# Optimization experiments

Hardware: AMD Instinct MI355X
Metric: run time of the kernel (lower is better)

The kernel has to match this reference:

```python
import jax, jax.numpy as jnp
import numpy as np
from math import factorial

L_MAX = 3
K = 256
N = 2048


def _cg_coeff(l1, m1, l2, m2, l3, m3):
    # Clebsch-Gordan coefficient <l1 m1 l2 m2 | l3 m3> via the Racah formula.
    if m3 != m1 + m2:
        return 0.0
    pref = ((2 * l3 + 1) * factorial(l3 + l1 - l2) * factorial(l3 - l1 + l2)
            * factorial(l1 + l2 - l3) / factorial(l1 + l2 + l3 + 1)) ** 0.5
    pref *= (factorial(l3 + m3) * factorial(l3 - m3) * factorial(l1 - m1)
             * factorial(l1 + m1) * factorial(l2 - m2) * factorial(l2 + m2)) ** 0.5
    s = 0.0
    for k in range(0, l1 + l2 - l3 + 1):
        d = [k, l1 + l2 - l3 - k, l1 - m1 - k, l2 + m2 - k,
             l3 - l2 + m1 + k, l3 - l1 - m2 + k]
        if min(d) < 0:
            continue
        den = 1.0
        for x in d:
            den *= factorial(x)
        s += (-1.0) ** k / den
    return pref * s


def _cg_tensor(l1, l2, l3):
    out = np.zeros((2 * l1 + 1, 2 * l2 + 1, 2 * l3 + 1), dtype=np.float32)
    for m1 in range(-l1, l1 + 1):
        for m2 in range(-l2, l2 + 1):
            m3 = m1 + m2
            if -l3 <= m3 <= l3:
                out[m1 + l1, m2 + l2, m3 + l3] = _cg_coeff(l1, m1, l2, m2, l3, m3)
    return jnp.asarray(out)


# All (l1, l2) -> l coupling paths allowed by the triangle inequality, l <= L_MAX.
PATHS = {l: [(l1, l2) for l1 in range(L_MAX + 1) for l2 in range(L_MAX + 1)
             if abs(l1 - l2) <= l <= l1 + l2] for l in range(L_MAX + 1)}
CG = {(l1, l2, l): _cg_tensor(l1, l2, l)
      for l in range(L_MAX + 1) for (l1, l2) in PATHS[l]}


def _forward(f1, f2, U, W):
    outs = []
    for l in range(L_MAX + 1):
        # CG tensor product: elementwise over channels k, coupled over (m1, m2) -> m.
        parts = [jnp.einsum('abm,nak,nbk->nmk', CG[(l1, l2, l)], f1[l1], f2[l2])
                 for (l1, l2) in PATHS[l]]
        tp = jnp.concatenate(parts, axis=-1)          # [N, 2l+1, n_paths(l)*K]
        mixed = jnp.einsum('nmc,ck->nmk', tp, U[l])   # U_dict per-l mixing -> [N, 2l+1, K]
        mixed = jnp.einsum('nmk,kj->nmj', mixed, W[l])  # learned per-l linear
        outs.append(f1[l] + mixed)                    # residual
    return tuple(outs)


def setup_inputs() -> dict:
    key = jax.random.key(0)
    ks = jax.random.split(key, 16)
    inp = {}
    for l in range(L_MAX + 1):
        inp[f'f1_l{l}'] = jax.random.normal(ks[l], (N, 2 * l + 1, K), jnp.float32)
        inp[f'f2_l{l}'] = jax.random.normal(ks[4 + l], (N, 2 * l + 1, K), jnp.float32)
        cin = len(PATHS[l]) * K
        inp[f'U_{l}'] = jax.random.normal(ks[8 + l], (cin, K), jnp.float32) / float(np.sqrt(cin))
        inp[f'W_{l}'] = jax.random.normal(ks[12 + l], (K, K), jnp.float32) / float(np.sqrt(K))
    return inp


def reference(f1_l0, f1_l1, f1_l2, f1_l3,
              f2_l0, f2_l1, f2_l2, f2_l3,
              U_0, U_1, U_2, U_3,
              W_0, W_1, W_2, W_3):
    f1 = [f1_l0, f1_l1, f1_l2, f1_l3]
    f2 = [f2_l0, f2_l1, f2_l2, f2_l3]
    U = [U_0, U_1, U_2, U_3]
    W = [W_0, W_1, W_2, W_3]
    return _forward(f1, f2, U, W)
```

## Files before the change

kernel.cpp:

```cpp
#include <hip/hip_runtime.h>
#include <math.h>

typedef __attribute__((ext_vector_type(4))) float f32x4;
typedef __attribute__((ext_vector_type(2))) float f32x2;
typedef __attribute__((ext_vector_type(8))) __bf16 bf16x8;
typedef __attribute__((ext_vector_type(4))) __bf16 bf16x4;
typedef __attribute__((ext_vector_type(2))) __bf16 bf16x2;

__device__ __constant__ int GP_L[34]  = {0,0,0,0, 1,1,1,1,1,1,1,1,1, 2,2,2,2,2,2,2,2,2,2,2, 3,3,3,3,3,3,3,3,3,3};
__device__ __constant__ int GP_L1[34] = {0,1,2,3, 0,1,1,1,2,2,2,3,3, 0,1,1,1,2,2,2,2,3,3,3, 0,1,1,2,2,2,3,3,3,3};
__device__ __constant__ int GP_L2[34] = {0,1,2,3, 1,0,1,2,1,2,3,2,3, 2,1,2,3,0,1,2,3,1,2,3, 3,2,3,1,2,3,0,1,2,3};

__device__ double dfact(int n) { double r = 1.0; for (int i = 2; i <= n; ++i) r *= (double)i; return r; }

__device__ double cg_coeff(int l1, int m1, int l2, int m2, int l3, int m3) {
  if (m3 != m1 + m2) return 0.0;
  double pref = sqrt((2.0 * l3 + 1.0) * dfact(l3 + l1 - l2) * dfact(l3 - l1 + l2)
                     * dfact(l1 + l2 - l3) / dfact(l1 + l2 + l3 + 1));
  pref *= sqrt(dfact(l3 + m3) * dfact(l3 - m3) * dfact(l1 - m1) * dfact(l1 + m1)
               * dfact(l2 - m2) * dfact(l2 + m2));
  double s = 0.0;
  for (int k = 0; k <= l1 + l2 - l3; ++k) {
    int d0 = k, d1 = l1 + l2 - l3 - k, d2 = l1 - m1 - k, d3 = l2 + m2 - k;
    int d4 = l3 - l2 + m1 + k, d5 = l3 - l1 - m2 + k;
    if (d0 < 0 || d1 < 0 || d2 < 0 || d3 < 0 || d4 < 0 || d5 < 0) continue;
    double den = dfact(d0) * dfact(d1) * dfact(d2) * dfact(d3) * dfact(d4) * dfact(d5);
    s += ((k & 1) ? -1.0 : 1.0) / den;
  }
  return pref * s;
}

__global__ __launch_bounds__(256) void prep(
    const float* __restrict__ u0, const float* __restrict__ u1,
    const float* __restrict__ u2, const float* __restrict__ u3,
    const float* __restrict__ w0, const float* __restrict__ w1,
    const float* __restrict__ w2, const float* __restrict__ w3,
    __bf16* __restrict__ Ubf, __bf16* __restrict__ Wt, float* __restrict__ cg) {
  const int bid = blockIdx.x, tid = threadIdx.x;
  if (bid < 2176) {
    long i = (long)bid * 256 + tid;
    const long b1 = 65536, b2 = 212992, b3 = 393216;
    const float* src; long s;
    if (i < b1)      { src = u0; s = i; }
    else if (i < b2) { src = u1; s = i - b1; }
    else if (i < b3) { src = u2; s = i - b2; }
    else             { src = u3; s = i - b3; }
    float4 v = ((const float4*)src)[s];
    bf16x4 o;
    o[0] = (__bf16)v.x; o[1] = (__bf16)v.y; o[2] = (__bf16)v.z; o[3] = (__bf16)v.w;
    ((bf16x4*)Ubf)[i] = o;
  } else if (bid < 3200) {
    int b = bid - 2176;
    int l = b >> 8, j = b & 255;
    const float* W = (l == 0) ? w0 : (l == 1) ? w1 : (l == 2) ? w2 : w3;
    Wt[((long)l << 16) + (j << 8) + tid] = (__bf16)W[(tid << 8) + j];
  } else {
    int idx = (bid - 3200) * 256 + tid;
    if (idx < 34 * 49) {
      int gp = idx / 49, r = idx % 49;
      int m1i = r / 7, m2i = r % 7;
      int l3 = GP_L[gp], l1 = GP_L1[gp], l2 = GP_L2[gp];
      float v = 0.f;
      if (m1i <= 2 * l1 && m2i <= 2 * l2) {
        int m1 = m1i - l1, m2 = m2i - l2, m3 = m1 + m2;
        if (m3 >= -l3 && m3 <= l3) v = (float)cg_coeff(l1, m1, l2, m2, l3, m3);
      }
      cg[idx] = v;
    }
  }
}

struct GemmDesc {
  const __bf16* A[4];
  const __bf16* B[4];
  __bf16*       C[4];
  int start[4];
  int lmap[4];
  int Kd[4];
  int Nc[4];
};

__device__ __forceinline__ void gload_lds16(const void* g, void* l) {
  __builtin_amdgcn_global_load_lds((const __attribute__((address_space(1))) void*)g,
                                   (__attribute__((address_space(3))) void*)l, 16, 0, 0);
}

__device__ void uw_body(const GemmDesc& d, int bid, char* sm) {
  const int tid = threadIdx.x;
  int seg = 0;
  if (bid >= d.start[1]) seg = 1;
  if (bid >= d.start[2]) seg = 2;
  if (bid >= d.start[3]) seg = 3;
  const int l = d.lmap[seg];
  const int rel = bid - d.start[seg];
  const int Kd = d.Kd[l], Nc = d.Nc[l];
  const int nTN = Nc >> 7;
  const int tM = rel / nTN, tN = rel % nTN;

  const int lane = tid & 63, wave = tid >> 6;
  const int wm = (wave >> 1) << 6, wn = (wave & 1) << 6;
  const int lr = lane & 15, lk = (lane >> 4) << 3;

  f32x4 acc[4][4] = {};

  const int r32 = tid >> 3;
  const int sl = ((tid & 7) ^ (r32 & 7)) << 3;
  const __bf16* Ag = d.A[l] + (long)(tM * 128 + r32) * Kd + sl;
  const __bf16* Bg = d.B[l] + (long)(tN * 128 + r32) * Kd + sl;
  char* AsB = sm;
  char* BsB = sm + 16384;

  for (int kt = 0; kt < Kd; kt += 64) {
#pragma unroll
    for (int i = 0; i < 4; ++i) {
      gload_lds16(Ag + (long)i * 32 * Kd + kt, AsB + i * 4096 + tid * 16);
      gload_lds16(Bg + (long)i * 32 * Kd + kt, BsB + i * 4096 + tid * 16);
    }
    __syncthreads();

#pragma unroll
    for (int kk = 0; kk < 64; kk += 32) {
      bf16x8 af[4], bq[4];
#pragma unroll
      for (int mi = 0; mi < 4; ++mi)
        af[mi] = *(const bf16x8*)(AsB + ((wm + mi * 16 + lr) << 7)
                                      + ((((kk + lk) << 1)) ^ ((lr & 7) << 4)));
#pragma unroll
      for (int ni = 0; ni < 4; ++ni)
        bq[ni] = *(const bf16x8*)(BsB + ((wn + ni * 16 + lr) << 7)
                                      + ((((kk + lk) << 1)) ^ ((lr & 7) << 4)));
#pragma unroll
      for (int mi = 0; mi < 4; ++mi)
#pragma unroll
        for (int ni = 0; ni < 4; ++ni)
          acc[mi][ni] = __builtin_amdgcn_mfma_f32_16x16x32_bf16(af[mi], bq[ni], acc[mi][ni], 0, 0, 0);
    }
    __syncthreads();
  }

  const long col0 = (long)tN * 128 + wn + lr;
  const long row0 = (long)tM * 128 + wm + ((lane >> 4) << 2);
#pragma unroll
  for (int mi = 0; mi < 4; ++mi)
#pragma unroll
    for (int j = 0; j < 4; ++j) {
      long r = row0 + mi * 16 + j;
      long base = r * (long)Nc + col0;
#pragma unroll
      for (int ni = 0; ni < 4; ++ni)
        d.C[l][base + ni * 16] = (__bf16)acc[mi][ni][j];
    }
}

#define TPW2(LV, DST, CIN, GOFF, P, L1V, L2V)                                    \
  { f32x2 tp[2 * (LV) + 1];                                                      \
    _Pragma("unroll") for (int m = 0; m <= 2 * (LV); ++m) { tp[m][0] = 0.f; tp[m][1] = 0.f; } \
    const float* cgt = cg + ((GOFF) + (P)) * 49;                                 \
    _Pragma("unroll") for (int a = 0; a <= 2 * (L1V); ++a)                       \
      _Pragma("unroll") for (int b = 0; b <= 2 * (L2V); ++b) {                   \
        const int m = a + b - ((L1V) + (L2V) - (LV));                            \
        if (m >= 0 && m <= 2 * (LV)) {                                           \
          float c = cgt[a * 7 + b];                                              \
          tp[m][0] = fmaf(c, v1[CUM[L1V] + a][0] * v2[CUM[L2V] + b][0], tp[m][0]); \
          tp[m][1] = fmaf(c, v1[CUM[L1V] + a][1] * v2[CUM[L2V] + b][1], tp[m][1]); \
        } }                                                                      \
    __bf16* o = (DST) + (n * (2 * (LV) + 1)) * (CIN) + (P) * 256 + k2;           \
    _Pragma("unroll") for (int m = 0; m <= 2 * (LV); ++m) {                      \
      bf16x2 ov; ov[0] = (__bf16)tp[m][0]; ov[1] = (__bf16)tp[m][1];             \
      *(bf16x2*)(o + (long)m * (CIN)) = ov; } }

template <int LMASK>
__device__ void tp_body(
    const float* __restrict__ f10, const float* __restrict__ f11,
    const float* __restrict__ f12, const float* __restrict__ f13,
    const float* __restrict__ f20, const float* __restrict__ f21,
    const float* __restrict__ f22, const float* __restrict__ f23,
    const float* __restrict__ cg,
    __bf16* __restrict__ A0, __bf16* __restrict__ A1,
    __bf16* __restrict__ A2, __bf16* __restrict__ A3, int bid) {
  const int tid = threadIdx.x;
  const long n = (long)bid * 2 + (tid >> 7);
  const int k2 = (tid & 127) << 1;
  constexpr int CUM[4] = {0, 1, 4, 9};
  const float* f1s[4] = {f10, f11, f12, f13};
  const float* f2s[4] = {f20, f21, f22, f23};

  f32x2 v1[16], v2[16];
#pragma unroll
  for (int l1 = 0; l1 < 4; ++l1) {
    const float* p1 = f1s[l1] + (n * (2 * l1 + 1)) * 256 + k2;
    const float* p2 = f2s[l1] + (n * (2 * l1 + 1)) * 256 + k2;
#pragma unroll
    for (int a = 0; a <= 2 * l1; ++a) {
      v1[CUM[l1] + a] = *(const f32x2*)(p1 + (long)a * 256);
      v2[CUM[l1] + a] = *(const f32x2*)(p2 + (long)a * 256);
    }
  }

  if constexpr (LMASK & 1) {
    TPW2(0, A0, 1024, 0, 0, 0, 0)  TPW2(0, A0, 1024, 0, 1, 1, 1)
    TPW2(0, A0, 1024, 0, 2, 2, 2)  TPW2(0, A0, 1024, 0, 3, 3, 3)
  }
  if constexpr (LMASK & 2) {
    TPW2(1, A1, 2304, 4, 0, 0, 1)  TPW2(1, A1, 2304, 4, 1, 1, 0)
    TPW2(1, A1, 2304, 4, 2, 1, 1)  TPW2(1, A1, 2304, 4, 3, 1, 2)
    TPW2(1, A1, 2304, 4, 4, 2, 1)  TPW2(1, A1, 2304, 4, 5, 2, 2)
    TPW2(1, A1, 2304, 4, 6, 2, 3)  TPW2(1, A1, 2304, 4, 7, 3, 2)
    TPW2(1, A1, 2304, 4, 8, 3, 3)
  }
  if constexpr (LMASK & 4) {
    TPW2(2, A2, 2816, 13, 0, 0, 2)  TPW2(2, A2, 2816, 13, 1, 1, 1)
    TPW2(2, A2, 2816, 13, 2, 1, 2)  TPW2(2, A2, 2816, 13, 3, 1, 3)
    TPW2(2, A2, 2816, 13, 4, 2, 0)  TPW2(2, A2, 2816, 13, 5, 2, 1)
    TPW2(2, A2, 2816, 13, 6, 2, 2)  TPW2(2, A2, 2816, 13, 7, 2, 3)
    TPW2(2, A2, 2816, 13, 8, 3, 1)  TPW2(2, A2, 2816, 13, 9, 3, 2)
    TPW2(2, A2, 2816, 13, 10, 3, 3)
  }
  if constexpr (LMASK & 8) {
    TPW2(3, A3, 2560, 24, 0, 0, 3)  TPW2(3, A3, 2560, 24, 1, 1, 2)
    TPW2(3, A3, 2560, 24, 2, 1, 3)  TPW2(3, A3, 2560, 24, 3, 2, 1)
    TPW2(3, A3, 2560, 24, 4, 2, 2)  TPW2(3, A3, 2560, 24, 5, 2, 3)
    TPW2(3, A3, 2560, 24, 6, 3, 0)  TPW2(3, A3, 2560, 24, 7, 3, 1)
    TPW2(3, A3, 2560, 24, 8, 3, 2)  TPW2(3, A3, 2560, 24, 9, 3, 3)
  }
}

template <int LMASK>
__global__ __launch_bounds__(256) void tp_uw(
    const float* __restrict__ f10, const float* __restrict__ f11,
    const float* __restrict__ f12, const float* __restrict__ f13,
    const float* __restrict__ f20, const float* __restrict__ f21,
    const float* __restrict__ f22, const float* __restrict__ f23,
    const float* __restrict__ cg,
    __bf16* __restrict__ A0, __bf16* __restrict__ A1,
    __bf16* __restrict__ A2, __bf16* __restrict__ A3,
    GemmDesc gd, int nUW) {
  __shared__ __align__(16) char sm[32768];
  const int bid = (int)blockIdx.x;
  if (bid < nUW) {
    uw_body(gd, bid, sm);
  } else if constexpr (LMASK != 0) {
    tp_body<LMASK>(f10, f11, f12, f13, f20, f21, f22, f23, cg,
                   A0, A1, A2, A3, bid - nUW);
  }
}

struct MainDesc {
  const __bf16* A[4];
  const __bf16* B[4];
  float*        C[4];
  const float*  R[4];
  int start[4];
  int lmap[4];
  int cin4[4];
};

__global__ __launch_bounds__(512, 4) void gemm_main(MainDesc d) {
  __shared__ __align__(16) char sm[49152];
  const int tid = threadIdx.x;
  int bid;
  {
    const int cpx = gridDim.x >> 3;
    bid = ((int)blockIdx.x & 7) * cpx + ((int)blockIdx.x >> 3);
  }
  int seg = 0;
  if (bid >= d.start[1]) seg = 1;
  if (bid >= d.start[2]) seg = 2;
  if (bid >= d.start[3]) seg = 3;
  const int l = d.lmap[seg];
  const int tM = bid - d.start[seg];
  const int cin = d.cin4[l];
  const int NT = cin >> 5;

  const __bf16* __restrict__ Aseg = d.A[l] + (long)tM * 128 * cin;
  const __bf16* __restrict__ Bseg = d.B[l];

  const int arow = tid >> 2;
  const int asx = (((tid & 3) ^ ((tid >> 3) & 3)) << 3);
  const int brow0 = tid >> 2;
  const int bsx0 = asx;
  const int brow1 = (512 + tid) >> 2;
  const int bsx1 = (((tid & 3) ^ (((512 + tid) >> 3) & 3)) << 3);

  const int lane = tid & 63, wave = tid >> 6;
  const int wm = (wave >> 2) << 6;
  const int wn = (wave & 3) << 6;
  const int lr = lane & 15;
  const int lslot = lane >> 4;

  f32x4 acc[4][4];
#pragma unroll
  for (int i = 0; i < 4; ++i)
#pragma unroll
    for (int j = 0; j < 4; ++j) { acc[i][j][0]=0.f; acc[i][j][1]=0.f; acc[i][j][2]=0.f; acc[i][j][3]=0.f; }

#define STAGE(s, t)                                                              \
  { char* base_ = sm + (s) * 24576;                                              \
    const long kt_ = (long)(t) << 5;                                             \
    gload_lds16(Aseg + (long)arow * cin + kt_ + asx, base_ + tid * 16);          \
    gload_lds16(Bseg + (long)brow0 * cin + kt_ + bsx0, base_ + 8192 + tid * 16); \
    gload_lds16(Bseg + (long)brow1 * cin + kt_ + bsx1, base_ + 8192 + 8192 + tid * 16); }

  STAGE(0, 0)
  __syncthreads();

  for (int t = 0; t < NT; ++t) {
    const int cur = t & 1;
    if (t + 1 < NT) STAGE(cur ^ 1, t + 1)
    const char* Ab = sm + cur * 24576;
    const char* Bb = Ab + 8192;
    bf16x8 af[4], bq[4];
#pragma unroll
    for (int mi = 0; mi < 4; ++mi) {
      const int row = wm + mi * 16 + lr;
      af[mi] = *(const bf16x8*)(Ab + row * 64 + ((lslot ^ ((row >> 1) & 3)) << 4));
    }
#pragma unroll
    for (int ni = 0; ni < 4; ++ni) {
      const int row = wn + ni * 16 + lr;
      bq[ni] = *(const bf16x8*)(Bb + row * 64 + ((lslot ^ ((row >> 1) & 3)) << 4));
    }
#pragma unroll
    for (int mi = 0; mi < 4; ++mi)
#pragma unroll
      for (int ni = 0; ni < 4; ++ni)
        acc[mi][ni] = __builtin_amdgcn_mfma_f32_16x16x32_bf16(af[mi], bq[ni], acc[mi][ni], 0, 0, 0);
    __syncthreads();
  }
#undef STAGE

  float* __restrict__ Cout = d.C[l];
  const float* __restrict__ Resid = d.R[l];
  const int rb = (lane >> 4) << 2;
#pragma unroll
  for (int mi = 0; mi < 4; ++mi)
#pragma unroll
    for (int j = 0; j < 4; ++j) {
      const long row = (long)tM * 128 + wm + mi * 16 + rb + j;
      const long base = row * 256 + wn + lr;
#pragma unroll
      for (int ni = 0; ni < 4; ++ni)
        Cout[base + ni * 16] = acc[mi][ni][j] + Resid[base + ni * 16];
    }
}

extern "C" void kernel_launch(void* const* d_in, const int* in_sizes, int n_in,
                              void* d_out, int out_size, void* d_ws, size_t ws_size,
                              hipStream_t stream) {
  const float* F1[4], * F2[4], * Uin[4], * Win[4];
  for (int l = 0; l < 4; ++l) {
    F1[l]  = (const float*)d_in[4 * l + 0];
    F2[l]  = (const float*)d_in[4 * l + 1];
    Uin[l] = (const float*)d_in[4 * l + 2];
    Win[l] = (const float*)d_in[4 * l + 3];
  }
  static const int  cin_[4]  = {1024, 2304, 2816, 2560};
  static const int  cum_[4]  = {0, 1024, 3328, 6144};
  static const long moff_[4] = {0, 524288, 2097152, 4718592};
  static const int  nTM_[4]  = {16, 48, 80, 112};
  static const long asz_[4]  = {4194304L, 28311552L, 57671680L, 73400320L};

  char* ws = (char*)d_ws;
  float*  cg   = (float*)ws;
  __bf16* Ubf  = (__bf16*)(ws + 8192);
  __bf16* Wtbf = (__bf16*)(ws + 8192 + 4456448);
  __bf16* UWt  = (__bf16*)(ws + 5242880);
  const long ABASE = 10485760;
  const bool big = ws_size >= (size_t)(ABASE + asz_[0] + asz_[1] + asz_[2] + asz_[3]);

  __bf16* Ab[4];
  if (big) {
    long off = ABASE;
    for (int l = 0; l < 4; ++l) { Ab[l] = (__bf16*)(ws + off); off += asz_[l]; }
  } else {
    for (int l = 0; l < 4; ++l) Ab[l] = (__bf16*)(ws + ABASE);
  }

  hipLaunchKernelGGL(prep, dim3(3207), dim3(256), 0, stream,
                     Uin[0], Uin[1], Uin[2], Uin[3],
                     Win[0], Win[1], Win[2], Win[3], Ubf, Wtbf, cg);

  GemmDesc gd;
  {
    int starts[4] = {0, 40, 84, 120};
    int lmap[4]   = {3, 2, 1, 0};
    for (int s = 0; s < 4; ++s) { gd.start[s] = starts[s]; gd.lmap[s] = lmap[s]; }
    for (int l = 0; l < 4; ++l) {
      gd.A[l] = Wtbf + (long)l * 65536;
      gd.B[l] = Ubf + (long)cum_[l] * 256;
      gd.C[l] = UWt + (long)cum_[l] * 256;
      gd.Kd[l] = 256;
      gd.Nc[l] = cin_[l];
    }
  }

  if (big) {
    hipLaunchKernelGGL((tp_uw<15>), dim3(1160), dim3(256), 0, stream,
                       F1[0], F1[1], F1[2], F1[3], F2[0], F2[1], F2[2], F2[3],
                       cg, Ab[0], Ab[1], Ab[2], Ab[3], gd, 136);
    MainDesc d;
    int starts[4] = {0, 112, 192, 240};
    int lmap[4]   = {3, 2, 1, 0};
    for (int s = 0; s < 4; ++s) { d.start[s] = starts[s]; d.lmap[s] = lmap[s]; }
    for (int l = 0; l < 4; ++l) {
      d.A[l] = Ab[l];
      d.B[l] = UWt + (long)cum_[l] * 256;
      d.C[l] = (float*)d_out + moff_[l];
      d.R[l] = F1[l];
      d.cin4[l] = cin_[l];
    }
    hipLaunchKernelGGL(gemm_main, dim3(256), dim3(512), 0, stream, d);
  } else {
    hipLaunchKernelGGL((tp_uw<0>), dim3(136), dim3(256), 0, stream,
                       F1[0], F1[1], F1[2], F1[3], F2[0], F2[1], F2[2], F2[3],
                       cg, Ab[0], Ab[1], Ab[2], Ab[3], gd, 136);
    for (int l = 0; l < 4; ++l) {
      switch (l) {
        case 0: hipLaunchKernelGGL((tp_uw<1>), dim3(1024), dim3(256), 0, stream,
                  F1[0],F1[1],F1[2],F1[3], F2[0],F2[1],F2[2],F2[3], cg,
                  Ab[0],Ab[1],Ab[2],Ab[3], gd, 0); break;
        case 1: hipLaunchKernelGGL((tp_uw<2>), dim3(1024), dim3(256), 0, stream,
                  F1[0],F1[1],F1[2],F1[3], F2[0],F2[1],F2[2],F2[3], cg,
                  Ab[0],Ab[1],Ab[2],Ab[3], gd, 0); break;
        case 2: hipLaunchKernelGGL((tp_uw<4>), dim3(1024), dim3(256), 0, stream,
                  F1[0],F1[1],F1[2],F1[3], F2[0],F2[1],F2[2],F2[3], cg,
                  Ab[0],Ab[1],Ab[2],Ab[3], gd, 0); break;
        case 3: hipLaunchKernelGGL((tp_uw<8>), dim3(1024), dim3(256), 0, stream,
                  F1[0],F1[1],F1[2],F1[3], F2[0],F2[1],F2[2],F2[3], cg,
                  Ab[0],Ab[1],Ab[2],Ab[3], gd, 0); break;
      }
      MainDesc d;
      for (int s = 0; s < 4; ++s) {
        d.start[s] = (s == 0) ? 0 : 0x7fffffff;
        d.lmap[s] = l;
      }
      for (int ll = 0; ll < 4; ++ll) {
        d.A[ll] = Ab[l];
        d.B[ll] = UWt + (long)cum_[l] * 256;
        d.C[ll] = (float*)d_out + moff_[l];
        d.R[ll] = F1[l];
        d.cin4[ll] = cin_[l];
      }
      hipLaunchKernelGGL(gemm_main, dim3(nTM_[l]), dim3(512), 0, stream, d);
    }
  }
  (void)in_sizes; (void)n_in; (void)out_size; (void)ws_size;
}
```

Measured before the change: 141.7 us.

## Retile main GEMM to 128x128 blocks with 64-deep K stages

The main GEMM moves from 128x256 output tiles on 512-thread blocks to 128x128 tiles on 256-thread blocks, splitting N across two blocks. The grid doubles from 256 to 512 blocks, which is meant to fill the 256 CUs better. Each pipeline stage now loads 64 K-elements with a new 8-way XOR swizzle, halving the number of K iterations and barriers. The cost is that each A tile is read twice from global memory, and each block uses 64 KB of LDS, which may limit how many blocks fit on a CU.

```diff
diff --git a/kernel.cpp b/kernel.cpp
--- a/kernel.cpp
+++ b/kernel.cpp
@@ -255,8 +255,8 @@
   int cin4[4];
 };
 
-__global__ __launch_bounds__(512, 4) void gemm_main(MainDesc d) {
-  __shared__ __align__(16) char sm[49152];
+__global__ __launch_bounds__(256) void gemm_main(MainDesc d) {
+  __shared__ __align__(16) char sm[65536];
   const int tid = threadIdx.x;
   int bid;
   {
@@ -268,25 +268,20 @@
   if (bid >= d.start[2]) seg = 2;
   if (bid >= d.start[3]) seg = 3;
   const int l = d.lmap[seg];
-  const int tM = bid - d.start[seg];
+  const int rel = bid - d.start[seg];
+  const int tM = rel >> 1, tN = rel & 1;
   const int cin = d.cin4[l];
-  const int NT = cin >> 5;
+  const int NT = cin >> 6;
 
   const __bf16* __restrict__ Aseg = d.A[l] + (long)tM * 128 * cin;
-  const __bf16* __restrict__ Bseg = d.B[l];
-
-  const int arow = tid >> 2;
-  const int asx = (((tid & 3) ^ ((tid >> 3) & 3)) << 3);
-  const int brow0 = tid >> 2;
-  const int bsx0 = asx;
-  const int brow1 = (512 + tid) >> 2;
-  const int bsx1 = (((tid & 3) ^ (((512 + tid) >> 3) & 3)) << 3);
+  const __bf16* __restrict__ Bseg = d.B[l] + (long)tN * 128 * cin;
+
+  const int r32 = tid >> 3;
+  const int sx = ((tid & 7) ^ (r32 & 7)) << 3;
 
   const int lane = tid & 63, wave = tid >> 6;
-  const int wm = (wave >> 2) << 6;
-  const int wn = (wave & 3) << 6;
-  const int lr = lane & 15;
-  const int lslot = lane >> 4;
+  const int wm = (wave >> 1) << 6, wn = (wave & 1) << 6;
+  const int lr = lane & 15, lkb = (lane >> 4) << 3;
 
   f32x4 acc[4][4];
 #pragma unroll
@@ -295,11 +290,15 @@
     for (int j = 0; j < 4; ++j) { acc[i][j][0]=0.f; acc[i][j][1]=0.f; acc[i][j][2]=0.f; acc[i][j][3]=0.f; }
 
 #define STAGE(s, t)                                                              \
-  { char* base_ = sm + (s) * 24576;                                              \
-    const long kt_ = (long)(t) << 5;                                             \
-    gload_lds16(Aseg + (long)arow * cin + kt_ + asx, base_ + tid * 16);          \
-    gload_lds16(Bseg + (long)brow0 * cin + kt_ + bsx0, base_ + 8192 + tid * 16); \
-    gload_lds16(Bseg + (long)brow1 * cin + kt_ + bsx1, base_ + 8192 + 8192 + tid * 16); }
+  { char* base_ = sm + (s) * 32768;                                              \
+    const long kt_ = (long)(t) << 6;                                             \
+    _Pragma("unroll")                                                            \
+    for (int i = 0; i < 4; ++i) {                                                \
+      gload_lds16(Aseg + (long)(i * 32 + r32) * cin + kt_ + sx,                  \
+                  base_ + i * 4096 + tid * 16);                                  \
+      gload_lds16(Bseg + (long)(i * 32 + r32) * cin + kt_ + sx,                  \
+                  base_ + 16384 + i * 4096 + tid * 16);                          \
+    } }
 
   STAGE(0, 0)
   __syncthreads();
@@ -307,24 +306,27 @@
   for (int t = 0; t < NT; ++t) {
     const int cur = t & 1;
     if (t + 1 < NT) STAGE(cur ^ 1, t + 1)
-    const char* Ab = sm + cur * 24576;
-    const char* Bb = Ab + 8192;
-    bf16x8 af[4], bq[4];
-#pragma unroll
-    for (int mi = 0; mi < 4; ++mi) {
-      const int row = wm + mi * 16 + lr;
-      af[mi] = *(const bf16x8*)(Ab + row * 64 + ((lslot ^ ((row >> 1) & 3)) << 4));
-    }
-#pragma unroll
-    for (int ni = 0; ni < 4; ++ni) {
-      const int row = wn + ni * 16 + lr;
-      bq[ni] = *(const bf16x8*)(Bb + row * 64 + ((lslot ^ ((row >> 1) & 3)) << 4));
-    }
-#pragma unroll
-    for (int mi = 0; mi < 4; ++mi)
-#pragma unroll
-      for (int ni = 0; ni < 4; ++ni)
-        acc[mi][ni] = __builtin_amdgcn_mfma_f32_16x16x32_bf16(af[mi], bq[ni], acc[mi][ni], 0, 0, 0);
+    const char* Ab = sm + cur * 32768;
+    const char* Bb = Ab + 16384;
+#pragma unroll
+    for (int kk = 0; kk < 64; kk += 32) {
+      bf16x8 af[4], bq[4];
+#pragma unroll
+      for (int mi = 0; mi < 4; ++mi) {
+        const int row = wm + mi * 16 + lr;
+        af[mi] = *(const bf16x8*)(Ab + (row << 7) + ((((kk + lkb) << 1)) ^ ((row & 7) << 4)));
+      }
+#pragma unroll
+      for (int ni = 0; ni < 4; ++ni) {
+        const int row = wn + ni * 16 + lr;
+        bq[ni] = *(const bf16x8*)(Bb + (row << 7) + ((((kk + lkb) << 1)) ^ ((row & 7) << 4)));
+      }
+#pragma unroll
+      for (int mi = 0; mi < 4; ++mi)
+#pragma unroll
+        for (int ni = 0; ni < 4; ++ni)
+          acc[mi][ni] = __builtin_amdgcn_mfma_f32_16x16x32_bf16(af[mi], bq[ni], acc[mi][ni], 0, 0, 0);
+    }
     __syncthreads();
   }
 #undef STAGE
@@ -337,7 +339,7 @@
 #pragma unroll
     for (int j = 0; j < 4; ++j) {
       const long row = (long)tM * 128 + wm + mi * 16 + rb + j;
-      const long base = row * 256 + wn + lr;
+      const long base = row * 256 + tN * 128 + wn + lr;
 #pragma unroll
       for (int ni = 0; ni < 4; ++ni)
         Cout[base + ni * 16] = acc[mi][ni][j] + Resid[base + ni * 16];
@@ -357,7 +359,7 @@
   static const int  cin_[4]  = {1024, 2304, 2816, 2560};
   static const int  cum_[4]  = {0, 1024, 3328, 6144};
   static const long moff_[4] = {0, 524288, 2097152, 4718592};
-  static const int  nTM_[4]  = {16, 48, 80, 112};
+  static const int  nBLK_[4] = {32, 96, 160, 224};
   static const long asz_[4]  = {4194304L, 28311552L, 57671680L, 73400320L};
 
   char* ws = (char*)d_ws;
@@ -399,7 +401,7 @@
                        F1[0], F1[1], F1[2], F1[3], F2[0], F2[1], F2[2], F2[3],
                        cg, Ab[0], Ab[1], Ab[2], Ab[3], gd, 136);
     MainDesc d;
-    int starts[4] = {0, 112, 192, 240};
+    int starts[4] = {0, 224, 384, 480};
     int lmap[4]   = {3, 2, 1, 0};
     for (int s = 0; s < 4; ++s) { d.start[s] = starts[s]; d.lmap[s] = lmap[s]; }
     for (int l = 0; l < 4; ++l) {
@@ -409,7 +411,7 @@
       d.R[l] = F1[l];
       d.cin4[l] = cin_[l];
     }
-    hipLaunchKernelGGL(gemm_main, dim3(256), dim3(512), 0, stream, d);
+    hipLaunchKernelGGL(gemm_main, dim3(512), dim3(256), 0, stream, d);
   } else {
     hipLaunchKernelGGL((tp_uw<0>), dim3(136), dim3(256), 0, stream,
                        F1[0], F1[1], F1[2], F1[3], F2[0], F2[1], F2[2], F2[3],
@@ -441,7 +443,7 @@
         d.R[ll] = F1[l];
         d.cin4[ll] = cin_[l];
       }
-      hipLaunchKernelGGL(gemm_main, dim3(nTM_[l]), dim3(512), 0, stream, d);
+      hipLaunchKernelGGL(gemm_main, dim3(nBLK_[l]), dim3(256), 0, stream, d);
     }
   }
   (void)in_sizes; (void)n_in; (void)out_size; (void)ws_size;
```

Measured after the change: 146.0 us. +3.1%, slower.
